# Optimization experiments

Hardware: AMD Instinct MI355X
Metric: run time of the kernel (lower is better)

The kernel has to match this reference:

```python
import jax, jax.numpy as jnp
import numpy as np

# db1 (Haar) analysis lowpass is [1/sqrt2, 1/sqrt2]; 2D separable LL kernel is
# all-ones 2x2 * 0.5 with stride 2. With 'zero' mode and even H,W there is no
# boundary contribution, so DWT LL == 2x2 block sum * 0.5.
# Inverse with all high-freq bands zeroed: each output pixel = LL * 0.5
# (1/sqrt2 per spatial dim), i.e. nearest-neighbor upsample of LL*0.5.

def _haar_ll(x):
    # x: [B, C, H, W] -> [B, C, H/2, W/2]
    B, C, H, W = x.shape
    return x.reshape(B, C, H // 2, 2, W // 2, 2).sum(axis=(3, 5)) * 0.5

def _haar_inv_ll(ll):
    # ll: [B, C, H, W] -> [B, C, 2H, 2W], details assumed zero
    B, C, H, W = ll.shape
    y = (ll * 0.5)[:, :, :, None, :, None]
    return jnp.broadcast_to(y, (B, C, H, 2, W, 2)).reshape(B, C, 2 * H, 2 * W)

def setup_inputs() -> dict:
    key = jax.random.key(0)
    image = jax.random.normal(key, (32768, 1, 28, 28), dtype=jnp.float32)
    return {"image": image, "lev": 2}

def reference(image, lev):
    # Batched equivalent of: per-sample DWTForward(J=lev, db1, zero) -> zero Yh
    # -> DWTInverse. lev is a static Python int.
    x = image
    for _ in range(lev):
        x = _haar_ll(x)
    for _ in range(lev):
        x = _haar_inv_ll(x)
    return x
```

## Files before the change

kernel.cpp:

```cpp
#include <hip/hip_runtime.h>


__global__ __launch_bounds__(256) void haar_ll2_kernel(
    const float* __restrict__ in, float* __restrict__ out, int total) {
    int tid = blockIdx.x * 256 + threadIdx.x;
    if (tid >= total) return;

    int img = tid / 49;
    int rem = tid - img * 49;
    int rg  = rem / 7;
    int cg  = rem - rg * 7;

    const float4* inp  = reinterpret_cast<const float4*>(in)  +
                         (size_t)img * 196 + rg * 28 + cg;
    float4*       outp = reinterpret_cast<float4*>(out) +
                         (size_t)img * 196 + rg * 28 + cg;

    float4 a = inp[0];
    float4 b = inp[7];
    float4 c = inp[14];
    float4 d = inp[21];

    float s = (a.x + a.y + a.z + a.w) + (b.x + b.y + b.z + b.w) +
              (c.x + c.y + c.z + c.w) + (d.x + d.y + d.z + d.w);
    s *= 0.0625f;

    float4 v = make_float4(s, s, s, s);
    outp[0]  = v;
    outp[7]  = v;
    outp[14] = v;
    outp[21] = v;
}

extern "C" void kernel_launch(void* const* d_in, const int* in_sizes, int n_in,
                              void* d_out, int out_size, void* d_ws, size_t ws_size,
                              hipStream_t stream) {
    const float* in  = (const float*)d_in[0];
    float*       out = (float*)d_out;
    int total  = in_sizes[0] / 16;
    int blocks = (total + 255) / 256;
    haar_ll2_kernel<<<blocks, 256, 0, stream>>>(in, out, total);
}
```

Before: 184.4 us.

## Stage float4 row sums in LDS for coalesced streaming of 16 images per block

Each block now handles 16 images. Threads load the input with fully contiguous float4 reads, reduce each float4 to a partial sum in shared memory, then after a barrier compute the 4x4 block averages from LDS and write contiguous float4 outputs. Before, each thread read and wrote four float4s strided by a row, so a wavefront's accesses were only partly contiguous. The change adds a block-wide barrier, 12.5 KB of LDS per block (which caps occupancy), and integer div/mod index math. It also assumes the image count is divisible by 16.

```diff
diff --git a/kernel.cpp b/kernel.cpp
--- a/kernel.cpp
+++ b/kernel.cpp
@@ -1,35 +1,38 @@
 #include <hip/hip_runtime.h>
 
 
-__global__ __launch_bounds__(256) void haar_ll2_kernel(
-    const float* __restrict__ in, float* __restrict__ out, int total) {
-    int tid = blockIdx.x * 256 + threadIdx.x;
-    if (tid >= total) return;
+__global__ __launch_bounds__(256) void haar_ll2_stream(
+    const float* __restrict__ in, float* __restrict__ out) {
+    __shared__ float P[3136];
+    const int tid = threadIdx.x;
+    const size_t base = (size_t)blockIdx.x * 3136;
+    const float4* __restrict__ in4  = reinterpret_cast<const float4*>(in)  + base;
+    float4*       __restrict__ out4 = reinterpret_cast<float4*>(out) + base;
 
-    int img = tid / 49;
-    int rem = tid - img * 49;
-    int rg  = rem / 7;
-    int cg  = rem - rg * 7;
+    #pragma unroll
+    for (int k = 0; k < 13; ++k) {
+        int f = tid + (k << 8);
+        if (f < 3136) {
+            float4 v = in4[f];
+            P[f] = (v.x + v.y) + (v.z + v.w);
+        }
+    }
+    __syncthreads();
 
-    const float4* inp  = reinterpret_cast<const float4*>(in)  +
-                         (size_t)img * 196 + rg * 28 + cg;
-    float4*       outp = reinterpret_cast<float4*>(out) +
-                         (size_t)img * 196 + rg * 28 + cg;
-
-    float4 a = inp[0];
-    float4 b = inp[7];
-    float4 c = inp[14];
-    float4 d = inp[21];
-
-    float s = (a.x + a.y + a.z + a.w) + (b.x + b.y + b.z + b.w) +
-              (c.x + c.y + c.z + c.w) + (d.x + d.y + d.z + d.w);
-    s *= 0.0625f;
-
-    float4 v = make_float4(s, s, s, s);
-    outp[0]  = v;
-    outp[7]  = v;
-    outp[14] = v;
-    outp[21] = v;
+    #pragma unroll
+    for (int k = 0; k < 13; ++k) {
+        int f = tid + (k << 8);
+        if (f < 3136) {
+            int img = f / 196;
+            int rem = f - img * 196;
+            int r   = rem / 7;
+            int cg  = rem - r * 7;
+            int rg  = r >> 2;
+            int a   = img * 196 + rg * 28 + cg;
+            float s = ((P[a] + P[a + 7]) + (P[a + 14] + P[a + 21])) * 0.0625f;
+            out4[f] = make_float4(s, s, s, s);
+        }
+    }
 }
 
 extern "C" void kernel_launch(void* const* d_in, const int* in_sizes, int n_in,
@@ -37,7 +40,6 @@
                               hipStream_t stream) {
     const float* in  = (const float*)d_in[0];
     float*       out = (float*)d_out;
-    int total  = in_sizes[0] / 16;
-    int blocks = (total + 255) / 256;
-    haar_ll2_kernel<<<blocks, 256, 0, stream>>>(in, out, total);
+    int nblocks = (in_sizes[0] / 784) / 16;
+    haar_ll2_stream<<<nblocks, 256, 0, stream>>>(in, out);
 }
```

New measurement: 184.5 us. About the same (+0.0%).
